# Kernel tuning notes

Measured on AMD Instinct MI355X. Metric: run time of the kernel, lower is better.

## Reference

```python
import jax, jax.numpy as jnp
import numpy as np

TRANSCRIBER_WEIGHT = 1.0
PREDICTOR_WEIGHT = 1.0


def setup_inputs() -> dict:
    key = jax.random.key(0)
    k1, k2, k3, k4 = jax.random.split(key, 4)
    B, T, U, D, V = 8, 256, 64, 512, 1024
    x = jax.random.normal(k1, (B, T, D), dtype=jnp.float32)   # transcriber output
    y = jax.random.normal(k2, (B, U, D), dtype=jnp.float32)   # predictor output
    # nn.Linear(D, V): weight [V, D], bias [V]
    W = jax.random.normal(k3, (V, D), dtype=jnp.float32) * (1.0 / np.sqrt(D))
    b = jax.random.normal(k4, (V,), dtype=jnp.float32) * 0.01
    return {"x": x, "y": y, "W": W, "b": b}


def reference(x, y, W, b):
    # h: [B, T, U, D] = tw * x[:, :, None, :] + pw * y[:, None, :, :]
    h = TRANSCRIBER_WEIGHT * x[:, :, None, :] + PREDICTOR_WEIGHT * y[:, None, :, :]
    h = jax.nn.relu(h)
    # linear: [B, T, U, V]
    return jnp.einsum('btud,vd->btuv', h, W) + b
```

## Files before the change

### kernel.cpp

```cpp
#include <hip/hip_runtime.h>
#include <hip/hip_bf16.h>


constexpr int Bc = 8, Tc = 256, Uc = 64, Dc = 512, Vc = 1024;
constexpr int BM = 64, BN = 512;
constexpr int NSTEPS = 16;
constexpr int BDIM = 512;

typedef __attribute__((ext_vector_type(8)))  short short8;
typedef __attribute__((ext_vector_type(8)))  unsigned short ushort8;
typedef __attribute__((ext_vector_type(4)))  float f32x4;
typedef __attribute__((ext_vector_type(16))) float f32x16;
typedef __attribute__((ext_vector_type(4)))  unsigned int u32x4;

__device__ inline unsigned short f2bf(float f) {
    union { float f; unsigned u; } v; v.f = f;
    unsigned r = v.u + 0x7FFFu + ((v.u >> 16) & 1u);
    return (unsigned short)(r >> 16);
}

__device__ inline unsigned int pkbf(float lo, float hi) {
    unsigned int r;
    asm("v_cvt_pk_bf16_f32 %0, %1, %2" : "=v"(r) : "v"(lo), "v"(hi));
    return r;
}

__global__ __launch_bounds__(256) void cvt_wt(const float* __restrict__ W,
                                              unsigned short* __restrict__ Wt) {
    const int idx  = blockIdx.x * 256 + threadIdx.x;
    const int v    = idx >> 6;
    const int koct = idx & 63;
    const float4 a = *(const float4*)(W + (size_t)v * Dc + koct * 8);
    const float4 b = *(const float4*)(W + (size_t)v * Dc + koct * 8 + 4);
    ushort8 o;
    o[0] = f2bf(a.x); o[1] = f2bf(a.y); o[2] = f2bf(a.z); o[3] = f2bf(a.w);
    o[4] = f2bf(b.x); o[5] = f2bf(b.y); o[6] = f2bf(b.z); o[7] = f2bf(b.w);
    const size_t chunk = (size_t)(koct >> 1) * 2048 + v * 2 + (koct & 1);
    *(ushort8*)(Wt + chunk * 8) = o;
}

__global__ __launch_bounds__(BDIM, 4) void joiner_v8(
    const float* __restrict__ x, const float* __restrict__ y,
    const unsigned short* __restrict__ Wt, const float* __restrict__ bias,
    float* __restrict__ out)
{
    __shared__ __align__(16) unsigned char smem[BM * Dc * 2];
    unsigned short* As = (unsigned short*)smem;

    const int tid  = threadIdx.x;
    const int lane = tid & 63;
    const int wid  = tid >> 6;
    const int l31  = lane & 31;
    const int l32  = lane >> 5;

    const int nhalf = blockIdx.x >> 11;
    const int mb    = blockIdx.x & 2047;
    const int bb    = mb >> 8;
    const int tt    = mb & 255;
    const int m0    = mb * BM;
    const int n0    = nhalf * BN;
    const int colbase = n0 + wid * 64;

    float bv[2];
    bv[0] = bias[colbase + l31];
    bv[1] = bias[colbase + 32 + l31];

    const unsigned short* pW = Wt + (size_t)(colbase * 2 + 2 * l31 + l32) * 8;

    short8 wfA[2][2], wfB[2][2];

    #define LOADW(buf, ks)                                                    \
        {                                                                     \
            _Pragma("unroll")                                                 \
            for (int q = 0; q < 2; ++q)                                       \
                _Pragma("unroll")                                             \
                for (int n16 = 0; n16 < 2; ++n16)                             \
                    buf[q][n16] = *(const short8*)(pW + ((ks) * 2 + q) * 16384 \
                                                   + n16 * 512);              \
        }

    LOADW(wfA, 0);

    const float* xrow = x + (size_t)(bb * Tc + tt) * Dc;
    #pragma unroll
    for (int i = 0; i < 8; ++i) {
        const int c = tid + i * BDIM;
        const int u = c >> 6;
        const int s = c & 63;
        const float4* xp = (const float4*)(xrow + s * 8);
        const float4* yp = (const float4*)(y + ((size_t)(bb * Uc + u) * Dc + s * 8));
        float4 xa = xp[0], xb = xp[1];
        float4 ya = yp[0], yb = yp[1];
        u32x4 pv;
        pv[0] = pkbf(fmaxf(xa.x + ya.x, 0.f), fmaxf(xa.y + ya.y, 0.f));
        pv[1] = pkbf(fmaxf(xa.z + ya.z, 0.f), fmaxf(xa.w + ya.w, 0.f));
        pv[2] = pkbf(fmaxf(xb.x + yb.x, 0.f), fmaxf(xb.y + yb.y, 0.f));
        pv[3] = pkbf(fmaxf(xb.z + yb.z, 0.f), fmaxf(xb.w + yb.w, 0.f));
        *(u32x4*)(&As[u * Dc + ((s ^ (u & 7)) * 8)]) = pv;
    }
    __syncthreads();

    f32x16 acc[2][2] = {};

    #define STEP(cur, nxt, ks)                                                \
        {                                                                     \
            if ((ks) + 1 < NSTEPS) LOADW(nxt, (ks) + 1);                      \
            _Pragma("unroll")                                                 \
            for (int q = 0; q < 2; ++q) {                                     \
                const int oA = (ks) * 4 + q * 2 + l32;                        \
                short8 af0 = *(const short8*)(&As[l31 * Dc                    \
                                              + ((oA ^ (l31 & 7)) * 8)]);     \
                short8 af1 = *(const short8*)(&As[(32 + l31) * Dc             \
                                              + ((oA ^ (l31 & 7)) * 8)]);     \
                __builtin_amdgcn_s_setprio(1);                                \
                acc[0][0] = __builtin_amdgcn_mfma_f32_32x32x16_bf16(          \
                    af0, cur[q][0], acc[0][0], 0, 0, 0);                      \
                acc[0][1] = __builtin_amdgcn_mfma_f32_32x32x16_bf16(          \
                    af0, cur[q][1], acc[0][1], 0, 0, 0);                      \
                acc[1][0] = __builtin_amdgcn_mfma_f32_32x32x16_bf16(          \
                    af1, cur[q][0], acc[1][0], 0, 0, 0);                      \
                acc[1][1] = __builtin_amdgcn_mfma_f32_32x32x16_bf16(          \
                    af1, cur[q][1], acc[1][1], 0, 0, 0);                      \
                __builtin_amdgcn_s_setprio(0);                                \
            }                                                                 \
        }

    #pragma unroll
    for (int ks = 0; ks < NSTEPS; ks += 2) {
        STEP(wfA, wfB, ks);
        STEP(wfB, wfA, ks + 1);
    }
    #undef STEP
    #undef LOADW

    __syncthreads();
    float* tr = (float*)smem + wid * (16 * 36);
    #pragma unroll
    for (int m16 = 0; m16 < 2; ++m16) {
        #pragma unroll
        for (int n16 = 0; n16 < 2; ++n16) {
            #pragma unroll
            for (int h = 0; h < 2; ++h) {
                #pragma unroll
                for (int e = 0; e < 8; ++e) {
                    const int rl = (e & 3) + 8 * (e >> 2) + 4 * l32;
                    tr[rl * 36 + l31] = acc[m16][n16][h * 8 + e] + bv[n16];
                }
                #pragma unroll
                for (int h2 = 0; h2 < 2; ++h2) {
                    const int rr = h2 * 8 + (lane >> 3);
                    const int c4 = (lane & 7) * 4;
                    f32x4 o;
                    o[0] = tr[rr * 36 + c4 + 0];
                    o[1] = tr[rr * 36 + c4 + 1];
                    o[2] = tr[rr * 36 + c4 + 2];
                    o[3] = tr[rr * 36 + c4 + 3];
                    const size_t off =
                        (size_t)(m0 + m16 * 32 + h * 16 + rr) * Vc
                        + colbase + n16 * 32 + c4;
                    __builtin_nontemporal_store(o, (f32x4*)(out + off));
                }
            }
        }
    }
}

constexpr int F_BM = 128, F_BN = 128, F_BK = 64;
constexpr int F_MT = (Bc * Tc * Uc) / F_BM;
constexpr int F_NT = Vc / F_BN;

__global__ __launch_bounds__(256) void joiner_mfma(
    const float* __restrict__ x, const float* __restrict__ y,
    const float* __restrict__ W, const float* __restrict__ bias,
    float* __restrict__ out)
{
    __shared__ unsigned short As[F_BM * F_BK];
    __shared__ unsigned short Wsh[F_BN * F_BK];
    const int tid = threadIdx.x;
    const int mtile = blockIdx.x % F_MT;
    const int ntile = blockIdx.x / F_MT;
    const int m0 = mtile * F_BM, v0 = ntile * F_BN;
    const int bb = m0 / (Tc * Uc);
    const int t0 = (m0 % (Tc * Uc)) / Uc;
    const int lane = tid & 63, wid = tid >> 6;
    const int wm = wid >> 1, wn = wid & 1;
    const int lr = lane & 15, lk8 = lane >> 4;
    f32x4 acc[4][4] = {};
    for (int k0 = 0; k0 < Dc; k0 += F_BK) {
        __syncthreads();
        #pragma unroll
        for (int i = 0; i < 4; ++i) {
            const int chunk = tid + i * 256;
            const int row = chunk >> 3, slot = chunk & 7;
            const int ps8 = (slot ^ (row & 7)) * 8;
            const int t = t0 + (row >> 6), u = row & 63;
            const float4* xp = (const float4*)(x + ((size_t)(bb * Tc + t) * Dc + k0 + slot * 8));
            const float4* yp = (const float4*)(y + ((size_t)(bb * Uc + u) * Dc + k0 + slot * 8));
            float4 xa = xp[0], xb2 = xp[1], ya = yp[0], yb2 = yp[1];
            ushort8 hv;
            hv[0] = f2bf(fmaxf(xa.x + ya.x, 0.f)); hv[1] = f2bf(fmaxf(xa.y + ya.y, 0.f));
            hv[2] = f2bf(fmaxf(xa.z + ya.z, 0.f)); hv[3] = f2bf(fmaxf(xa.w + ya.w, 0.f));
            hv[4] = f2bf(fmaxf(xb2.x + yb2.x, 0.f)); hv[5] = f2bf(fmaxf(xb2.y + yb2.y, 0.f));
            hv[6] = f2bf(fmaxf(xb2.z + yb2.z, 0.f)); hv[7] = f2bf(fmaxf(xb2.w + yb2.w, 0.f));
            *(ushort8*)(&As[row * F_BK + ps8]) = hv;
            const float4* wp = (const float4*)(W + ((size_t)(v0 + row) * Dc + k0 + slot * 8));
            float4 wa = wp[0], wb2 = wp[1];
            ushort8 wv;
            wv[0] = f2bf(wa.x); wv[1] = f2bf(wa.y); wv[2] = f2bf(wa.z); wv[3] = f2bf(wa.w);
            wv[4] = f2bf(wb2.x); wv[5] = f2bf(wb2.y); wv[6] = f2bf(wb2.z); wv[7] = f2bf(wb2.w);
            *(ushort8*)(&Wsh[row * F_BK + ps8]) = wv;
        }
        __syncthreads();
        #pragma unroll
        for (int kk = 0; kk < 2; ++kk) {
            const int psk = kk * 4 + lk8;
            short8 af[4], bfr[4];
            #pragma unroll
            for (int mf = 0; mf < 4; ++mf) {
                const int row = wm * 64 + mf * 16 + lr;
                af[mf] = *(const short8*)(&As[row * F_BK + ((psk ^ (row & 7)) * 8)]);
            }
            #pragma unroll
            for (int nf = 0; nf < 4; ++nf) {
                const int row = wn * 64 + nf * 16 + lr;
                bfr[nf] = *(const short8*)(&Wsh[row * F_BK + ((psk ^ (row & 7)) * 8)]);
            }
            #pragma unroll
            for (int mf = 0; mf < 4; ++mf)
                #pragma unroll
                for (int nf = 0; nf < 4; ++nf)
                    acc[mf][nf] = __builtin_amdgcn_mfma_f32_16x16x32_bf16(af[mf], bfr[nf], acc[mf][nf], 0, 0, 0);
        }
    }
    #pragma unroll
    for (int nf = 0; nf < 4; ++nf) {
        const int v = v0 + wn * 64 + nf * 16 + lr;
        const float bv = bias[v];
        #pragma unroll
        for (int mf = 0; mf < 4; ++mf) {
            const int mrow = m0 + wm * 64 + mf * 16 + (lane >> 4) * 4;
            #pragma unroll
            for (int j = 0; j < 4; ++j)
                out[(size_t)(mrow + j) * Vc + v] = acc[mf][nf][j] + bv;
        }
    }
}

extern "C" void kernel_launch(void* const* d_in, const int* in_sizes, int n_in,
                              void* d_out, int out_size, void* d_ws, size_t ws_size,
                              hipStream_t stream) {
    const float* x = (const float*)d_in[0];
    const float* y = (const float*)d_in[1];
    const float* W = (const float*)d_in[2];
    const float* b = (const float*)d_in[3];
    float* out = (float*)d_out;

    const size_t w_bytes = (size_t)Vc * Dc * sizeof(unsigned short);
    if (ws_size >= w_bytes) {
        unsigned short* Wt = (unsigned short*)d_ws;
        cvt_wt<<<dim3((Vc * Dc / 8) / 256), 256, 0, stream>>>(W, Wt);
        joiner_v8<<<dim3((Bc * Tc * Uc / BM) * (Vc / BN)), BDIM, 0, stream>>>(x, y, Wt, b, out);
    } else {
        joiner_mfma<<<dim3(F_MT * F_NT), 256, 0, stream>>>(x, y, W, b, out);
    }
}
```

Baseline: 184.6 us.

## Make joiner kernel persistent over eight M tiles per block

Each block now processes eight consecutive 64-row M tiles in a loop instead of one. The grid shrinks by a factor of eight, and block indices are interleaved so the two N halves of the same rows run on adjacent blocks. This amortises block launch and setup cost and the per-block bias load. In exchange, staging of the next A tile is serialized between the output store and the next GEMM, adding extra barriers without overlap, and the smaller grid may reduce load balance and occupancy.

Result: slower. 670.6 us (+263.2%).

```diff
diff --git a/kernel.cpp b/kernel.cpp
--- a/kernel.cpp
+++ b/kernel.cpp
@@ -6,6 +6,7 @@
 constexpr int BM = 64, BN = 512;
 constexpr int NSTEPS = 16;
 constexpr int BDIM = 512;
+constexpr int TILES = 8;
 
 typedef __attribute__((ext_vector_type(8)))  short short8;
 typedef __attribute__((ext_vector_type(8)))  unsigned short ushort8;
@@ -39,7 +40,7 @@
     *(ushort8*)(Wt + chunk * 8) = o;
 }
 
-__global__ __launch_bounds__(BDIM, 4) void joiner_v8(
+__global__ __launch_bounds__(BDIM, 4) void joiner_v9(
     const float* __restrict__ x, const float* __restrict__ y,
     const unsigned short* __restrict__ Wt, const float* __restrict__ bias,
     float* __restrict__ out)
@@ -53,11 +54,8 @@
     const int l31  = lane & 31;
     const int l32  = lane >> 5;
 
-    const int nhalf = blockIdx.x >> 11;
-    const int mb    = blockIdx.x & 2047;
-    const int bb    = mb >> 8;
-    const int tt    = mb & 255;
-    const int m0    = mb * BM;
+    const int nhalf = blockIdx.x & 1;
+    const int mbase = (blockIdx.x >> 1) * TILES;
     const int n0    = nhalf * BN;
     const int colbase = n0 + wid * 64;
 
@@ -79,28 +77,28 @@
                                                    + n16 * 512);              \
         }
 
-    LOADW(wfA, 0);
-
-    const float* xrow = x + (size_t)(bb * Tc + tt) * Dc;
-    #pragma unroll
-    for (int i = 0; i < 8; ++i) {
-        const int c = tid + i * BDIM;
-        const int u = c >> 6;
-        const int s = c & 63;
-        const float4* xp = (const float4*)(xrow + s * 8);
-        const float4* yp = (const float4*)(y + ((size_t)(bb * Uc + u) * Dc + s * 8));
-        float4 xa = xp[0], xb = xp[1];
-        float4 ya = yp[0], yb = yp[1];
-        u32x4 pv;
-        pv[0] = pkbf(fmaxf(xa.x + ya.x, 0.f), fmaxf(xa.y + ya.y, 0.f));
-        pv[1] = pkbf(fmaxf(xa.z + ya.z, 0.f), fmaxf(xa.w + ya.w, 0.f));
-        pv[2] = pkbf(fmaxf(xb.x + yb.x, 0.f), fmaxf(xb.y + yb.y, 0.f));
-        pv[3] = pkbf(fmaxf(xb.z + yb.z, 0.f), fmaxf(xb.w + yb.w, 0.f));
-        *(u32x4*)(&As[u * Dc + ((s ^ (u & 7)) * 8)]) = pv;
-    }
-    __syncthreads();
-
-    f32x16 acc[2][2] = {};
+    #define STAGE(jj)                                                         \
+        {                                                                     \
+            const int mb_ = mbase + (jj);                                     \
+            const float* xrow_ = x + (size_t)((mb_ >> 8) * Tc + (mb_ & 255)) * Dc; \
+            const float* yb_   = y + (size_t)(mb_ >> 8) * Uc * Dc;            \
+            _Pragma("unroll")                                                 \
+            for (int i = 0; i < 8; ++i) {                                     \
+                const int c = tid + i * BDIM;                                 \
+                const int u = c >> 6;                                         \
+                const int s = c & 63;                                         \
+                const float4* xp = (const float4*)(xrow_ + s * 8);            \
+                const float4* yp = (const float4*)(yb_ + (size_t)u * Dc + s * 8); \
+                float4 xa = xp[0], xb = xp[1];                                \
+                float4 ya = yp[0], yb2 = yp[1];                               \
+                u32x4 pv;                                                     \
+                pv[0] = pkbf(fmaxf(xa.x + ya.x, 0.f), fmaxf(xa.y + ya.y, 0.f)); \
+                pv[1] = pkbf(fmaxf(xa.z + ya.z, 0.f), fmaxf(xa.w + ya.w, 0.f)); \
+                pv[2] = pkbf(fmaxf(xb.x + yb2.x, 0.f), fmaxf(xb.y + yb2.y, 0.f)); \
+                pv[3] = pkbf(fmaxf(xb.z + yb2.z, 0.f), fmaxf(xb.w + yb2.w, 0.f)); \
+                *(u32x4*)(&As[u * Dc + ((s ^ (u & 7)) * 8)]) = pv;            \
+            }                                                                 \
+        }
 
     #define STEP(cur, nxt, ks)                                                \
         {                                                                     \
@@ -125,44 +123,62 @@
             }                                                                 \
         }
 
-    #pragma unroll
-    for (int ks = 0; ks < NSTEPS; ks += 2) {
-        STEP(wfA, wfB, ks);
-        STEP(wfB, wfA, ks + 1);
-    }
-    #undef STEP
-    #undef LOADW
-
+    LOADW(wfA, 0);
+    STAGE(0);
     __syncthreads();
-    float* tr = (float*)smem + wid * (16 * 36);
-    #pragma unroll
-    for (int m16 = 0; m16 < 2; ++m16) {
-        #pragma unroll
-        for (int n16 = 0; n16 < 2; ++n16) {
-            #pragma unroll
-            for (int h = 0; h < 2; ++h) {
+
+    #pragma unroll 1
+    for (int j = 0; j < TILES; ++j) {
+        const int m0 = (mbase + j) * BM;
+
+        f32x16 acc[2][2] = {};
+        #pragma unroll
+        for (int ks = 0; ks < NSTEPS; ks += 2) {
+            STEP(wfA, wfB, ks);
+            STEP(wfB, wfA, ks + 1);
+        }
+        if (j + 1 < TILES) LOADW(wfA, 0);
+        __syncthreads();
+
+        float* tr = (float*)smem + wid * (16 * 36);
+        #pragma unroll
+        for (int m16 = 0; m16 < 2; ++m16) {
+            #pragma unroll
+            for (int n16 = 0; n16 < 2; ++n16) {
                 #pragma unroll
-                for (int e = 0; e < 8; ++e) {
-                    const int rl = (e & 3) + 8 * (e >> 2) + 4 * l32;
-                    tr[rl * 36 + l31] = acc[m16][n16][h * 8 + e] + bv[n16];
-                }
-                #pragma unroll
-                for (int h2 = 0; h2 < 2; ++h2) {
-                    const int rr = h2 * 8 + (lane >> 3);
-                    const int c4 = (lane & 7) * 4;
-                    f32x4 o;
-                    o[0] = tr[rr * 36 + c4 + 0];
-                    o[1] = tr[rr * 36 + c4 + 1];
-                    o[2] = tr[rr * 36 + c4 + 2];
-                    o[3] = tr[rr * 36 + c4 + 3];
-                    const size_t off =
-                        (size_t)(m0 + m16 * 32 + h * 16 + rr) * Vc
-                        + colbase + n16 * 32 + c4;
-                    __builtin_nontemporal_store(o, (f32x4*)(out + off));
+                for (int h = 0; h < 2; ++h) {
+                    #pragma unroll
+                    for (int e = 0; e < 8; ++e) {
+                        const int rl = (e & 3) + 8 * (e >> 2) + 4 * l32;
+                        tr[rl * 36 + l31] = acc[m16][n16][h * 8 + e] + bv[n16];
+                    }
+                    #pragma unroll
+                    for (int h2 = 0; h2 < 2; ++h2) {
+                        const int rr = h2 * 8 + (lane >> 3);
+                        const int c4 = (lane & 7) * 4;
+                        f32x4 o;
+                        o[0] = tr[rr * 36 + c4 + 0];
+                        o[1] = tr[rr * 36 + c4 + 1];
+                        o[2] = tr[rr * 36 + c4 + 2];
+                        o[3] = tr[rr * 36 + c4 + 3];
+                        const size_t off =
+                            (size_t)(m0 + m16 * 32 + h * 16 + rr) * Vc
+                            + colbase + n16 * 32 + c4;
+                        __builtin_nontemporal_store(o, (f32x4*)(out + off));
+                    }
                 }
             }
         }
-    }
+
+        if (j + 1 < TILES) {
+            __syncthreads();
+            STAGE(j + 1);
+            __syncthreads();
+        }
+    }
+    #undef STEP
+    #undef STAGE
+    #undef LOADW
 }
 
 constexpr int F_BM = 128, F_BN = 128, F_BK = 64;
@@ -259,7 +275,7 @@
     if (ws_size >= w_bytes) {
         unsigned short* Wt = (unsigned short*)d_ws;
         cvt_wt<<<dim3((Vc * Dc / 8) / 256), 256, 0, stream>>>(W, Wt);
-        joiner_v8<<<dim3((Bc * Tc * Uc / BM) * (Vc / BN)), BDIM, 0, stream>>>(x, y, Wt, b, out);
+        joiner_v9<<<dim3((Bc * Tc * Uc / BM / TILES) * (Vc / BN)), BDIM, 0, stream>>>(x, y, Wt, b, out);
     } else {
         joiner_mfma<<<dim3(F_MT * F_NT), 256, 0, stream>>>(x, y, W, b, out);
     }
```
